# Optimization experiments

Hardware: AMD Instinct MI355X
Metric: run time of the kernel (lower is better)

## Reference

```python
import jax, jax.numpy as jnp
import numpy as np

N, D, NUM_CLASSES = 1024, 256, 10
EPS = 1e-12


def setup_inputs() -> dict:
    key = jax.random.key(0)
    k1, k2, k3, k4 = jax.random.split(key, 4)
    return {
        "fm_s": jax.random.normal(k1, (N, D), dtype=jnp.float32),
        "fm_t": jax.random.normal(k2, (N, D), dtype=jnp.float32),
        "logvar_s": jax.random.normal(k3, (N, D), dtype=jnp.float32),
        "targets": jax.random.randint(k4, (N,), 0, NUM_CLASSES, dtype=jnp.int64),
        "fusion_true": 0,  # False branch (no multi_index)
    }


def reference(fm_s, fm_t, logvar_s, targets, fusion_true):
    # pairwise squared diff scaled by per-row (student) variance: (N, N, D)
    diff2 = (fm_s[:, None, :] - fm_t[None, :, :]) ** 2
    inv_var_term = diff2 / (2.0 * jnp.exp(logvar_s)[:, None, :] + EPS)
    half_lv = 0.5 * logvar_s[:, None, :]
    lp = jax.nn.relu(inv_var_term + half_lv).sum(-1)   # (N, N)
    ln = jax.nn.relu(-inv_var_term - half_lv).sum(-1)  # (N, N)
    pos = (targets[:, None] == targets[None, :]).astype(fm_s.dtype)  # self_mask_pos
    neg = 1.0 - pos
    loss_pos = lp * pos / pos.sum(-1, keepdims=True)
    loss_neg = ln * neg / neg.sum(-1, keepdims=True)
    # fusion_true == False path
    return loss_pos.sum(-1).mean() + loss_neg.sum(-1).mean()
```

## Files before the change

### kernel.cpp

```cpp
#include <hip/hip_runtime.h>
#include <math.h>

#define NN   1024
#define DD   256
#define NCLS 10

#define TI 64
#define TJ 128
#define DC 32
#define DSPLIT 8
#define NBLK ((NN / TI) * (NN / TJ) * DSPLIT)

typedef float f32x2 __attribute__((ext_vector_type(2)));
typedef float f32x4 __attribute__((ext_vector_type(4)));

__global__ __launch_bounds__(256) void count_kernel(const long long* __restrict__ tgt,
                                                    int* __restrict__ counts) {
    __shared__ int c[NCLS];
    int tid = threadIdx.x;
    if (tid < NCLS) c[tid] = 0;
    __syncthreads();
    for (int k = tid; k < NN; k += 256) atomicAdd(&c[(int)tgt[k]], 1);
    __syncthreads();
    if (tid < NCLS) counts[tid] = c[tid];
}

__global__ __launch_bounds__(256) void pair_kernel(
    const float* __restrict__ fm_s, const float* __restrict__ fm_t,
    const float* __restrict__ lv, const long long* __restrict__ tgt,
    const int* __restrict__ counts, float* __restrict__ partials)
{
    __shared__ float Al[TI * DC];
    __shared__ float Bl[TI * DC];
    __shared__ float Vl[TI * DC];
    __shared__ float Fl[TJ * DC];

    const int bid  = blockIdx.x;
    const int tile = bid >> 3;
    const int kd   = bid & 7;
    const int i0   = (tile >> 3) * TI;
    const int j0   = (tile & 7) * TJ;
    const int doff = kd * DC;

    const int tid  = threadIdx.x;
    const int tx   = tid & 15;
    const int ty   = tid >> 4;
    const int lane = tid & 63;
    const int w    = tid >> 6;

    const int srow = tid >> 3;
    const int sq   = tid & 7;
#pragma unroll
    for (int p = 0; p < 4; ++p) {
        const int r = p * 32 + srow;
        f32x4 v = *(const f32x4*)&fm_t[(j0 + r) * DD + doff + sq * 4];
        const int phys = (sq + (r >> 3)) & 7;
        *(f32x4*)&Fl[r * DC + phys * 4] = v;
    }
#pragma unroll
    for (int p = 0; p < 2; ++p) {
        const int r = p * 32 + srow;
        const int g = (i0 + r) * DD + doff + sq * 4;
        f32x4 fs = *(const f32x4*)&fm_s[g];
        f32x4 l  = *(const f32x4*)&lv[g];
        f32x4 A, B, V;
#pragma unroll
        for (int e = 0; e < 4; ++e) {
            const float iv = 0.5f * __expf(-l[e]);
            const float fsiv = fs[e] * iv;
            A[e] = fmaf(fsiv, fs[e], 0.5f * l[e]);
            B[e] = -2.0f * fsiv;
            V[e] = iv;
        }
        const int phys = (sq + (r >> 2)) & 7;
        *(f32x4*)&Al[r * DC + phys * 4] = A;
        *(f32x4*)&Bl[r * DC + phys * 4] = B;
        *(f32x4*)&Vl[r * DC + phys * 4] = V;
    }

    const int* tgt32 = (const int*)tgt;
    int ti_r[4], tj_r[8];
    float wp_r[4], wn_r[4];
#pragma unroll
    for (int ri = 0; ri < 4; ++ri) {
        ti_r[ri] = tgt32[(i0 + ty * 4 + ri) * 2];
        const int cnt = counts[ti_r[ri]];
        wp_r[ri] = 1.0f / (float)cnt;
        wn_r[ri] = 1.0f / (float)(NN - cnt);
    }
#pragma unroll
    for (int rj = 0; rj < 8; ++rj) tj_r[rj] = tgt32[(j0 + tx * 8 + rj) * 2];

    __syncthreads();

    f32x2 s1v[4][8];
    float s2[4][8];
#pragma unroll
    for (int a = 0; a < 4; ++a)
#pragma unroll
        for (int b = 0; b < 8; ++b) { s1v[a][b] = (f32x2)(0.f); s2[a][b] = 0.f; }

#pragma unroll
    for (int k = 0; k < 8; ++k) {
        const int iq = ((k + ty) & 7) * 4;
        const f32x4* pa = (const f32x4*)&Al[ty * 128 + iq];
        const f32x4* pb = (const f32x4*)&Bl[ty * 128 + iq];
        const f32x4* pv = (const f32x4*)&Vl[ty * 128 + iq];
        f32x4 fa[4], fb[4], fv[4];
#pragma unroll
        for (int r = 0; r < 4; ++r) {
            fa[r] = pa[r * 8];
            fb[r] = pb[r * 8];
            fv[r] = pv[r * 8];
        }
        const f32x4* pf = (const f32x4*)&Fl[tx * 256 + ((k + tx) & 7) * 4];
#pragma unroll
        for (int rj = 0; rj < 8; ++rj) {
            const f32x4 f = pf[rj * 8];
            const f32x2 f01 = f.lo, f23 = f.hi;
            const f32x2 g01 = f01 * f01, g23 = f23 * f23;
#pragma unroll
            for (int ri = 0; ri < 4; ++ri) {
                const f32x2 t01 = __builtin_elementwise_fma(g01, fv[ri].lo,
                                    __builtin_elementwise_fma(f01, fb[ri].lo, fa[ri].lo));
                const f32x2 t23 = __builtin_elementwise_fma(g23, fv[ri].hi,
                                    __builtin_elementwise_fma(f23, fb[ri].hi, fa[ri].hi));
                s1v[ri][rj] += (t01 + t23);
                s2[ri][rj] += (fabsf(t01.x) + fabsf(t01.y))
                            + (fabsf(t23.x) + fabsf(t23.y));
            }
        }
    }

    float csum = 0.f;
#pragma unroll
    for (int ri = 0; ri < 4; ++ri) {
#pragma unroll
        for (int rj = 0; rj < 8; ++rj) {
            const float s1 = s1v[ri][rj].x + s1v[ri][rj].y;
            const float lp = 0.5f * (s2[ri][rj] + s1);
            const float ln = 0.5f * (s2[ri][rj] - s1);
            csum += (ti_r[ri] == tj_r[rj]) ? lp * wp_r[ri] : ln * wn_r[ri];
        }
    }

#pragma unroll
    for (int off = 32; off > 0; off >>= 1) csum += __shfl_down(csum, off);
    __syncthreads();
    if (lane == 0) Al[w] = csum;
    __syncthreads();
    if (tid == 0) partials[bid] = (Al[0] + Al[1]) + (Al[2] + Al[3]);
}

__global__ __launch_bounds__(256) void finalize_kernel(const float* __restrict__ partials,
                                                       float* __restrict__ out) {
    __shared__ float red[256];
    const int tid = threadIdx.x;
    red[tid] = (partials[tid] + partials[tid + 256]) +
               (partials[tid + 512] + partials[tid + 768]);
    __syncthreads();
    for (int s = 128; s > 0; s >>= 1) {
        if (tid < s) red[tid] += red[tid + s];
        __syncthreads();
    }
    if (tid == 0) out[0] = red[0] * (1.0f / (float)NN);
}

extern "C" void kernel_launch(void* const* d_in, const int* in_sizes, int n_in,
                              void* d_out, int out_size, void* d_ws, size_t ws_size,
                              hipStream_t stream) {
    const float* fm_s    = (const float*)d_in[0];
    const float* fm_t    = (const float*)d_in[1];
    const float* lv      = (const float*)d_in[2];
    const long long* tgt = (const long long*)d_in[3];

    int*   counts   = (int*)d_ws;
    float* partials = (float*)((char*)d_ws + 64);

    hipLaunchKernelGGL(count_kernel, dim3(1), dim3(256), 0, stream, tgt, counts);
    hipLaunchKernelGGL(pair_kernel, dim3(NBLK), dim3(256), 0, stream,
                       fm_s, fm_t, lv, tgt, counts, partials);
    hipLaunchKernelGGL(finalize_kernel, dim3(1), dim3(256), 0, stream,
                       partials, (float*)d_out);
}
```

Measured before the change: 36.94 us.

## Fold class counting into pair kernel and hand-issue packed FMA math

Drops the separate count kernel. Each pair block now builds its own class histogram in shared memory with LDS atomics, which removes one launch and its serial dependency. The inner loop is rewritten with inline v_pk_fma_f32 and v_pk_add_f32 asm in Horner form, so the f*f product is gone. Target loads move to the epilogue to reduce register pressure. In exchange, every block re-counts all 1024 targets, and the inline asm hides the code from compiler scheduling.

```diff
diff --git a/kernel.cpp b/kernel.cpp
--- a/kernel.cpp
+++ b/kernel.cpp
@@ -14,26 +14,23 @@
 typedef float f32x2 __attribute__((ext_vector_type(2)));
 typedef float f32x4 __attribute__((ext_vector_type(4)));
 
-__global__ __launch_bounds__(256) void count_kernel(const long long* __restrict__ tgt,
-                                                    int* __restrict__ counts) {
-    __shared__ int c[NCLS];
-    int tid = threadIdx.x;
-    if (tid < NCLS) c[tid] = 0;
-    __syncthreads();
-    for (int k = tid; k < NN; k += 256) atomicAdd(&c[(int)tgt[k]], 1);
-    __syncthreads();
-    if (tid < NCLS) counts[tid] = c[tid];
-}
+#define PK_FMA(d, a, b, c) \
+    asm("v_pk_fma_f32 %0, %1, %2, %3" : "=v"(d) : "v"(a), "v"(b), "v"(c))
+#define PK_ADD(d, a, b) \
+    asm("v_pk_add_f32 %0, %1, %2" : "=v"(d) : "v"(a), "v"(b))
+#define PK_ACC(acc, x) \
+    asm("v_pk_add_f32 %0, %0, %1" : "+v"(acc) : "v"(x))
 
 __global__ __launch_bounds__(256) void pair_kernel(
     const float* __restrict__ fm_s, const float* __restrict__ fm_t,
     const float* __restrict__ lv, const long long* __restrict__ tgt,
-    const int* __restrict__ counts, float* __restrict__ partials)
+    float* __restrict__ partials)
 {
     __shared__ float Al[TI * DC];
     __shared__ float Bl[TI * DC];
     __shared__ float Vl[TI * DC];
     __shared__ float Fl[TJ * DC];
+    __shared__ int   ch[16];
 
     const int bid  = blockIdx.x;
     const int tile = bid >> 3;
@@ -47,6 +44,10 @@
     const int ty   = tid >> 4;
     const int lane = tid & 63;
     const int w    = tid >> 6;
+
+    const int* tgt32 = (const int*)tgt;
+
+    if (tid < 16) ch[tid] = 0;
 
     const int srow = tid >> 3;
     const int sq   = tid & 7;
@@ -78,18 +79,10 @@
         *(f32x4*)&Vl[r * DC + phys * 4] = V;
     }
 
-    const int* tgt32 = (const int*)tgt;
-    int ti_r[4], tj_r[8];
-    float wp_r[4], wn_r[4];
+    __syncthreads();
 #pragma unroll
-    for (int ri = 0; ri < 4; ++ri) {
-        ti_r[ri] = tgt32[(i0 + ty * 4 + ri) * 2];
-        const int cnt = counts[ti_r[ri]];
-        wp_r[ri] = 1.0f / (float)cnt;
-        wn_r[ri] = 1.0f / (float)(NN - cnt);
-    }
-#pragma unroll
-    for (int rj = 0; rj < 8; ++rj) tj_r[rj] = tgt32[(j0 + tx * 8 + rj) * 2];
+    for (int k = 0; k < 4; ++k)
+        atomicAdd(&ch[tgt32[(k * 256 + tid) * 2]], 1);
 
     __syncthreads();
 
@@ -118,14 +111,15 @@
         for (int rj = 0; rj < 8; ++rj) {
             const f32x4 f = pf[rj * 8];
             const f32x2 f01 = f.lo, f23 = f.hi;
-            const f32x2 g01 = f01 * f01, g23 = f23 * f23;
 #pragma unroll
             for (int ri = 0; ri < 4; ++ri) {
-                const f32x2 t01 = __builtin_elementwise_fma(g01, fv[ri].lo,
-                                    __builtin_elementwise_fma(f01, fb[ri].lo, fa[ri].lo));
-                const f32x2 t23 = __builtin_elementwise_fma(g23, fv[ri].hi,
-                                    __builtin_elementwise_fma(f23, fb[ri].hi, fa[ri].hi));
-                s1v[ri][rj] += (t01 + t23);
+                f32x2 u01, u23, t01, t23, st;
+                PK_FMA(u01, fv[ri].lo, f01, fb[ri].lo);
+                PK_FMA(u23, fv[ri].hi, f23, fb[ri].hi);
+                PK_FMA(t01, u01, f01, fa[ri].lo);
+                PK_FMA(t23, u23, f23, fa[ri].hi);
+                PK_ADD(st, t01, t23);
+                PK_ACC(s1v[ri][rj], st);
                 s2[ri][rj] += (fabsf(t01.x) + fabsf(t01.y))
                             + (fabsf(t23.x) + fabsf(t23.y));
             }
@@ -135,12 +129,17 @@
     float csum = 0.f;
 #pragma unroll
     for (int ri = 0; ri < 4; ++ri) {
+        const int t   = tgt32[(i0 + ty * 4 + ri) * 2];
+        const int cnt = ch[t];
+        const float wp = 1.0f / (float)cnt;
+        const float wn = 1.0f / (float)(NN - cnt);
 #pragma unroll
         for (int rj = 0; rj < 8; ++rj) {
+            const int tj = tgt32[(j0 + tx * 8 + rj) * 2];
             const float s1 = s1v[ri][rj].x + s1v[ri][rj].y;
             const float lp = 0.5f * (s2[ri][rj] + s1);
             const float ln = 0.5f * (s2[ri][rj] - s1);
-            csum += (ti_r[ri] == tj_r[rj]) ? lp * wp_r[ri] : ln * wn_r[ri];
+            csum += (t == tj) ? lp * wp : ln * wn;
         }
     }
 
@@ -174,12 +173,10 @@
     const float* lv      = (const float*)d_in[2];
     const long long* tgt = (const long long*)d_in[3];
 
-    int*   counts   = (int*)d_ws;
-    float* partials = (float*)((char*)d_ws + 64);
+    float* partials = (float*)d_ws;
 
-    hipLaunchKernelGGL(count_kernel, dim3(1), dim3(256), 0, stream, tgt, counts);
     hipLaunchKernelGGL(pair_kernel, dim3(NBLK), dim3(256), 0, stream,
-                       fm_s, fm_t, lv, tgt, counts, partials);
+                       fm_s, fm_t, lv, tgt, partials);
     hipLaunchKernelGGL(finalize_kernel, dim3(1), dim3(256), 0, stream,
                        partials, (float*)d_out);
 }
```

Measured after the change: 39.34 us. 6.5% more time.
